# Kernel optimization log

Measured on AMD Instinct MI355X. Metric: run time of the kernel, lower is better.

## Reference

```python
import jax, jax.numpy as jnp
import numpy as np

N = 12288   # num_nodes
D = 128     # isize
K_TOP = 31  # k + 1, per top_k(similarities, self.k + 1)


def setup_inputs() -> dict:
    key = jax.random.key(0)
    features = jax.random.normal(key, (N, D), dtype=jnp.float32)
    eye = jnp.eye(D, dtype=jnp.float32)  # param_init: weight <- I, bias <- 0
    return {
        "features": features,
        "W1": eye,
        "b1": jnp.zeros((D,), jnp.float32),
        "W2": eye,
        "b2": jnp.zeros((D,), jnp.float32),
    }


def reference(features, W1, b1, W2, b2):
    # internal_forward: Linear -> ReLU -> Linear (nlayers=2, act='relu')
    h = jax.nn.relu(features @ W1.T + b1)
    h = h @ W2.T + b2
    # F.normalize(h, dim=1, p=2) with eps=1e-12
    hn = h / jnp.maximum(jnp.linalg.norm(h, axis=1, keepdims=True), 1e-12)
    # dense N x N cosine similarity
    sim = hn @ hn.T
    # top_k: keep top (k+1) entries per row, zero elsewhere; then apply_non_linearity='relu'
    vals, idx = jax.lax.top_k(sim, K_TOP)          # [N, K_TOP]
    rows = jnp.arange(sim.shape[0])[:, None]       # [N, 1]
    # relu(sim * mask) == scatter relu(top-k values) into a zero matrix
    out = jnp.zeros_like(sim).at[rows, idx].set(jax.nn.relu(vals))
    return out
```

## Files before the change

kernel.cpp:

```cpp
#include <hip/hip_runtime.h>
#include <stdint.h>
#include <math.h>

#define NN 12288
#define DD 128
#define KTOP 31
#define TILE 128
#define GB (NN / TILE)
#define TCAND 64
#define CCAP 128

typedef __attribute__((ext_vector_type(8))) short bf16x8;
typedef __attribute__((ext_vector_type(4))) float f32x4;

__device__ __forceinline__ unsigned short f2bf(float x) {
  unsigned int u = __float_as_uint(x);
  u += 0x7fffu + ((u >> 16) & 1u);
  return (unsigned short)(u >> 16);
}

__global__ __launch_bounds__(128)
void mlp_norm_kernel(const float* __restrict__ feat,
                     const float* __restrict__ W1, const float* __restrict__ b1,
                     const float* __restrict__ W2, const float* __restrict__ b2,
                     double* __restrict__ hn64, unsigned short* __restrict__ hnb) {
  __shared__ double bufA[8][DD];
  __shared__ double bufB[8][DD];
  __shared__ double mnorm[8];
  const int t = threadIdx.x;
  const int row0 = blockIdx.x * 8;

  #pragma unroll
  for (int rr = 0; rr < 8; ++rr)
    bufA[rr][t] = (double)feat[(size_t)(row0 + rr) * DD + t];
  __syncthreads();

  {
    double acc[8] = {0,0,0,0,0,0,0,0};
    const float* wrow = W1 + (size_t)t * DD;
    for (int k = 0; k < DD; ++k) {
      double w = (double)wrow[k];
      #pragma unroll
      for (int rr = 0; rr < 8; ++rr)
        acc[rr] = fma(w, bufA[rr][k], acc[rr]);
    }
    double bb = (double)b1[t];
    #pragma unroll
    for (int rr = 0; rr < 8; ++rr)
      bufB[rr][t] = fmax(acc[rr] + bb, 0.0);
  }
  __syncthreads();
  {
    double acc[8] = {0,0,0,0,0,0,0,0};
    const float* wrow = W2 + (size_t)t * DD;
    for (int k = 0; k < DD; ++k) {
      double w = (double)wrow[k];
      #pragma unroll
      for (int rr = 0; rr < 8; ++rr)
        acc[rr] = fma(w, bufB[rr][k], acc[rr]);
    }
    double bb = (double)b2[t];
    #pragma unroll
    for (int rr = 0; rr < 8; ++rr)
      bufA[rr][t] = acc[rr] + bb;
  }
  __syncthreads();

  const int lane = t & 63;
  const int w = t >> 6;
  #pragma unroll
  for (int r2 = 0; r2 < 4; ++r2) {
    int rr = w * 4 + r2;
    double x0 = bufA[rr][lane];
    double x1 = bufA[rr][lane + 64];
    double s = x0 * x0 + x1 * x1;
    #pragma unroll
    for (int d = 1; d < 64; d <<= 1)
      s += __shfl_xor(s, d);
    if (lane == 0) mnorm[rr] = fmax(sqrt(s), 1e-12);
  }
  __syncthreads();
  #pragma unroll
  for (int rr = 0; rr < 8; ++rr) {
    double v = bufA[rr][t] / mnorm[rr];
    hn64[(size_t)(row0 + rr) * DD + t] = v;
    hnb[(size_t)(row0 + rr) * DD + t] = f2bf((float)v);
  }
}

__device__ __forceinline__ int lunit(int c, int r, int q) {
  return c * 512 + r * 4 + ((q + (r >> 1)) & 3);
}

__global__ __launch_bounds__(256)
void gemm_kernel(const unsigned short* __restrict__ hnb,
                 unsigned short* __restrict__ simmat) {
  __shared__ __attribute__((aligned(16))) unsigned short At[16384];
  __shared__ __attribute__((aligned(16))) unsigned short Bt[16384];
  const int t = threadIdx.x;
  const int lane = t & 63;
  const int wv = t >> 6;
  const int bi = blockIdx.x / GB, bj = blockIdx.x % GB;
  const int r0 = bi * TILE, c0 = bj * TILE;

  #pragma unroll
  for (int i = 0; i < 8; ++i) {
    int u = i * 256 + t;
    int c = u >> 9, r = (u >> 2) & 127, g = u & 3;
    int q = (g - (r >> 1)) & 3;
    uint4 v = *(const uint4*)(hnb + (size_t)(r0 + r) * DD + c * 32 + q * 8);
    *(uint4*)(At + u * 8) = v;
  }
  #pragma unroll
  for (int i = 0; i < 8; ++i) {
    int u = i * 256 + t;
    int c = u >> 9, r = (u >> 2) & 127, g = u & 3;
    int q = (g - (r >> 1)) & 3;
    uint4 v = *(const uint4*)(hnb + (size_t)(c0 + r) * DD + c * 32 + q * 8);
    *(uint4*)(Bt + u * 8) = v;
  }
  __syncthreads();

  const int wr = (wv >> 1) * 64;
  const int wc = (wv & 1) * 64;
  const int m = lane & 15, quad = lane >> 4;

  f32x4 acc[4][4] = {};
  #pragma unroll
  for (int kc = 0; kc < 4; ++kc) {
    bf16x8 a[4], b[4];
    #pragma unroll
    for (int i = 0; i < 4; ++i)
      a[i] = *(const bf16x8*)(At + lunit(kc, wr + i * 16 + m, quad) * 8);
    #pragma unroll
    for (int j = 0; j < 4; ++j)
      b[j] = *(const bf16x8*)(Bt + lunit(kc, wc + j * 16 + m, quad) * 8);
    #pragma unroll
    for (int i = 0; i < 4; ++i)
      #pragma unroll
      for (int j = 0; j < 4; ++j)
        acc[i][j] = __builtin_amdgcn_mfma_f32_16x16x32_bf16(a[i], b[j], acc[i][j], 0, 0, 0);
  }

  const bool evenl = !(lane & 1);
  #pragma unroll
  for (int i = 0; i < 4; ++i)
    #pragma unroll
    for (int j = 0; j < 4; ++j)
      #pragma unroll
      for (int r = 0; r < 4; ++r) {
        float v = acc[i][j][r];
        float v2 = __shfl_xor(v, 1);
        if (evenl) {
          unsigned int pk = (unsigned int)f2bf(v) | ((unsigned int)f2bf(v2) << 16);
          int R = r0 + wr + i * 16 + quad * 4 + r;
          int C = c0 + wc + j * 16 + m;
          *(unsigned int*)(simmat + (size_t)R * NN + C) = pk;
        }
      }
}

#define PINS(P) { \
  unsigned p_ = (P); \
  _Pragma("unroll") \
  for (int i_ = 0; i_ < 7; ++i_) \
    L[i_] = (p_ > L[i_ + 1]) ? L[i_ + 1] : (L[i_] > p_ ? L[i_] : p_); \
  L[7] = L[7] > p_ ? L[7] : p_; }

__global__ __launch_bounds__(256)
void scan_rescore_kernel(const unsigned short* __restrict__ simmat,
                         const double* __restrict__ hn64,
                         float* __restrict__ resval, int* __restrict__ rescol) {
  __shared__ unsigned scand[4][CCAP];
  const int t = threadIdx.x, lane = t & 63, wv = t >> 6;
  const int row = blockIdx.x * 4 + wv;
  const unsigned short* srow = simmat + (size_t)row * NN;

  unsigned L[8] = {0, 0, 0, 0, 0, 0, 0, 0};
  for (int it = 0; it < NN / 512; ++it) {
    uint4 pk = *(const uint4*)(srow + it * 512 + lane * 8);
    const unsigned cb = it * 512 + lane * 8;
    unsigned wds[4] = {pk.x, pk.y, pk.z, pk.w};
    #pragma unroll
    for (int q = 0; q < 4; ++q) {
      unsigned b0 = wds[q] & 0xFFFFu, b1 = wds[q] >> 16;
      unsigned s0 = (b0 & 0x8000u) ? 0u : b0;
      unsigned s1 = (b1 & 0x8000u) ? 0u : b1;
      unsigned p0 = (s0 << 16) | (cb + 2 * q);
      unsigned p1 = (s1 << 16) | (cb + 2 * q + 1);
      if (p0 > L[0]) { PINS(p0) }
      if (p1 > L[0]) { PINS(p1) }
    }
  }

  unsigned lo = 0, hi = 0xFFFFu;
  while (lo < hi) {
    unsigned mid = (lo + hi + 1) >> 1;
    int c = 0;
    #pragma unroll
    for (int i = 0; i < 8; ++i) c += (int)((L[i] >> 16) >= mid);
    #pragma unroll
    for (int d = 1; d < 64; d <<= 1) c += __shfl_xor(c, d);
    if (c >= TCAND) lo = mid; else hi = mid - 1;
  }
  const unsigned thr = lo;

  int cl = 0;
  #pragma unroll
  for (int i = 0; i < 8; ++i) cl += (int)((L[i] >> 16) >= thr);
  int pre = cl;
  #pragma unroll
  for (int d = 1; d < 64; d <<= 1) {
    int y = __shfl_up(pre, d);
    if (lane >= d) pre += y;
  }
  const int total = __shfl(pre, 63);
  const int nc = total < CCAP ? total : CCAP;
  int slot = pre - cl;
  #pragma unroll
  for (int i = 0; i < 8; ++i) {
    if ((L[i] >> 16) >= thr) {
      if (slot < CCAP) scand[wv][slot] = L[i];
      ++slot;
    }
  }
  __syncthreads();

  const double* arow = hn64 + (size_t)row * DD;
  double rv0 = -1.0e300, rv1 = -1.0e300;
  int rc0 = 0x7fffffff, rc1 = 0x7fffffff;
  if (lane < nc) {
    const int col = (int)(scand[wv][lane] & 0xFFFFu);
    const double* brow = hn64 + (size_t)col * DD;
    double acc = 0.0;
    for (int k = 0; k < DD; k += 2) {
      double2 a2 = *(const double2*)(arow + k);
      double2 b2 = *(const double2*)(brow + k);
      acc = fma(a2.x, b2.x, acc);
      acc = fma(a2.y, b2.y, acc);
    }
    rv0 = acc; rc0 = col;
  }
  if (lane + 64 < nc) {
    const int col = (int)(scand[wv][lane + 64] & 0xFFFFu);
    const double* brow = hn64 + (size_t)col * DD;
    double acc = 0.0;
    for (int k = 0; k < DD; k += 2) {
      double2 a2 = *(const double2*)(arow + k);
      double2 b2 = *(const double2*)(brow + k);
      acc = fma(a2.x, b2.x, acc);
      acc = fma(a2.y, b2.y, acc);
    }
    rv1 = acc; rc1 = col;
  }

  for (int itk = 0; itk < KTOP; ++itk) {
    bool f = (rv0 > rv1) || (rv0 == rv1 && rc0 < rc1);
    double bv = f ? rv0 : rv1;
    int bc = f ? rc0 : rc1;
    #pragma unroll
    for (int d = 1; d < 64; d <<= 1) {
      double ov = __shfl_xor(bv, d);
      int    oc = __shfl_xor(bc, d);
      bool tk = (ov > bv) || (ov == bv && oc < bc);
      bv = tk ? ov : bv;
      bc = tk ? oc : bc;
    }
    if (lane == itk) {
      resval[(size_t)row * KTOP + itk] = (float)fmax(bv, 0.0);
      rescol[(size_t)row * KTOP + itk] = bc;
    }
    if (rv0 == bv && rc0 == bc) rv0 = -1.0e300;
    else if (rv1 == bv && rc1 == bc) rv1 = -1.0e300;
  }
}

__global__ __launch_bounds__(256)
void emit_kernel(const float* __restrict__ resval, const int* __restrict__ rescol,
                 float* __restrict__ out) {
  const int row = blockIdx.x, t = threadIdx.x;
  float v = 0.0f; int c = 0;
  if (t < KTOP) {
    v = resval[(size_t)row * KTOP + t];
    c = rescol[(size_t)row * KTOP + t];
  }
  float4* orow = (float4*)(out + (size_t)row * NN);
  const float4 z = {0.0f, 0.0f, 0.0f, 0.0f};
  #pragma unroll
  for (int i = 0; i < NN / 4 / 256; ++i)
    orow[i * 256 + t] = z;
  __syncthreads();
  if (t < KTOP) out[(size_t)row * NN + c] = v;
}

extern "C" void kernel_launch(void* const* d_in, const int* in_sizes, int n_in,
                              void* d_out, int out_size, void* d_ws, size_t ws_size,
                              hipStream_t stream) {
  const float* feat = (const float*)d_in[0];
  const float* W1 = (const float*)d_in[1];
  const float* b1 = (const float*)d_in[2];
  const float* W2 = (const float*)d_in[3];
  const float* b2 = (const float*)d_in[4];
  float* out = (float*)d_out;

  double* hn64 = (double*)d_ws;
  unsigned short* hnb = (unsigned short*)(hn64 + (size_t)NN * DD);
  float* resval = (float*)(hnb + (size_t)NN * DD);
  int* rescol = (int*)(resval + (size_t)NN * KTOP);

  unsigned short* simmat = (unsigned short*)d_out;

  mlp_norm_kernel<<<NN / 8, 128, 0, stream>>>(feat, W1, b1, W2, b2, hn64, hnb);
  gemm_kernel<<<GB * GB, 256, 0, stream>>>(hnb, simmat);
  scan_rescore_kernel<<<NN / 4, 256, 0, stream>>>(simmat, hn64, resval, rescol);
  emit_kernel<<<NN, 256, 0, stream>>>(resval, rescol, out);
}
```

Measured before the change: 1.025 ms.

## Filter similarity tiles in GEMM epilogue using per-row sampled thresholds

Adds a tau kernel that, for each row, computes similarities against a 512-row sample and takes the 24th-largest as a lower-bound threshold. The GEMM epilogue now appends only entries above that threshold to a per-row candidate buffer via atomics, instead of writing the full bf16 similarity matrix. The rescore kernel then reads these small candidate lists rather than scanning full rows. This removes the large simmat write and read traffic, at the cost of an extra kernel, atomic contention, and a fixed candidate capacity that could overflow or, if the sampled threshold is loose, miss true top-k entries.

```diff
diff --git a/kernel.cpp b/kernel.cpp
--- a/kernel.cpp
+++ b/kernel.cpp
@@ -9,6 +9,9 @@
 #define GB (NN / TILE)
 #define TCAND 64
 #define CCAP 128
+#define CAP 1536
+#define TAUN 512
+#define TAURANK 24
 
 typedef __attribute__((ext_vector_type(8))) short bf16x8;
 typedef __attribute__((ext_vector_type(4))) float f32x4;
@@ -17,6 +20,9 @@
   unsigned int u = __float_as_uint(x);
   u += 0x7fffu + ((u >> 16) & 1u);
   return (unsigned short)(u >> 16);
+}
+__device__ __forceinline__ float bf2f(unsigned int us) {
+  return __uint_as_float((us & 0xFFFFu) << 16);
 }
 
 __global__ __launch_bounds__(128)
@@ -88,13 +94,59 @@
   }
 }
 
+__global__ __launch_bounds__(256)
+void tau_kernel(const unsigned short* __restrict__ hnb,
+                unsigned short* __restrict__ tau) {
+  __shared__ unsigned short rowbuf[4 * DD];
+  const int t = threadIdx.x, lane = t & 63, wv = t >> 6;
+  const int row0 = blockIdx.x * 4;
+  ((unsigned*)rowbuf)[t] = ((const unsigned*)(hnb + (size_t)row0 * DD))[t];
+  __syncthreads();
+  const unsigned short* rb = rowbuf + wv * DD;
+
+  float acc[8] = {0,0,0,0,0,0,0,0};
+  for (int k8 = 0; k8 < DD; k8 += 8) {
+    float rv[8];
+    #pragma unroll
+    for (int e = 0; e < 8; ++e) rv[e] = bf2f(rb[k8 + e]);
+    #pragma unroll
+    for (int s = 0; s < 8; ++s) {
+      uint4 cv = *(const uint4*)(hnb + (size_t)(lane + 64 * s) * DD + k8);
+      unsigned wd[4] = {cv.x, cv.y, cv.z, cv.w};
+      #pragma unroll
+      for (int q = 0; q < 4; ++q) {
+        acc[s] = fmaf(bf2f(wd[q]), rv[2 * q], acc[s]);
+        acc[s] = fmaf(bf2f(wd[q] >> 16), rv[2 * q + 1], acc[s]);
+      }
+    }
+  }
+  unsigned key[8];
+  #pragma unroll
+  for (int s = 0; s < 8; ++s) {
+    unsigned bf = f2bf(acc[s]);
+    key[s] = (bf & 0x8000u) ? 0u : bf;
+  }
+  unsigned lo = 0, hi = 0xFFFFu;
+  while (lo < hi) {
+    unsigned mid = (lo + hi + 1) >> 1;
+    int c = 0;
+    #pragma unroll
+    for (int s = 0; s < 8; ++s) c += (int)(key[s] >= mid);
+    #pragma unroll
+    for (int d = 1; d < 64; d <<= 1) c += __shfl_xor(c, d);
+    if (c >= TAURANK) lo = mid; else hi = mid - 1;
+  }
+  if (lane == 0) tau[row0 + wv] = (unsigned short)(lo ? lo - 1 : 0);
+}
+
 __device__ __forceinline__ int lunit(int c, int r, int q) {
   return c * 512 + r * 4 + ((q + (r >> 1)) & 3);
 }
 
 __global__ __launch_bounds__(256)
-void gemm_kernel(const unsigned short* __restrict__ hnb,
-                 unsigned short* __restrict__ simmat) {
+void gemm_filter_kernel(const unsigned short* __restrict__ hnb,
+                        const unsigned short* __restrict__ tau,
+                        int* __restrict__ cnt, unsigned* __restrict__ cand) {
   __shared__ __attribute__((aligned(16))) unsigned short At[16384];
   __shared__ __attribute__((aligned(16))) unsigned short Bt[16384];
   const int t = threadIdx.x;
@@ -142,7 +194,13 @@
         acc[i][j] = __builtin_amdgcn_mfma_f32_16x16x32_bf16(a[i], b[j], acc[i][j], 0, 0, 0);
   }
 
-  const bool evenl = !(lane & 1);
+  unsigned short tr[4][4];
+  #pragma unroll
+  for (int i = 0; i < 4; ++i)
+    #pragma unroll
+    for (int r = 0; r < 4; ++r)
+      tr[i][r] = tau[r0 + wr + i * 16 + quad * 4 + r];
+
   #pragma unroll
   for (int i = 0; i < 4; ++i)
     #pragma unroll
@@ -150,47 +208,32 @@
       #pragma unroll
       for (int r = 0; r < 4; ++r) {
         float v = acc[i][j][r];
-        float v2 = __shfl_xor(v, 1);
-        if (evenl) {
-          unsigned int pk = (unsigned int)f2bf(v) | ((unsigned int)f2bf(v2) << 16);
+        unsigned bf = f2bf(v);
+        unsigned key = (bf & 0x8000u) ? 0u : bf;
+        if (key >= (unsigned)tr[i][r]) {
           int R = r0 + wr + i * 16 + quad * 4 + r;
           int C = c0 + wc + j * 16 + m;
-          *(unsigned int*)(simmat + (size_t)R * NN + C) = pk;
+          int idx = atomicAdd(&cnt[R], 1);
+          if (idx < CAP) cand[(size_t)R * CAP + idx] = (key << 16) | (unsigned)C;
         }
       }
 }
 
-#define PINS(P) { \
-  unsigned p_ = (P); \
-  _Pragma("unroll") \
-  for (int i_ = 0; i_ < 7; ++i_) \
-    L[i_] = (p_ > L[i_ + 1]) ? L[i_ + 1] : (L[i_] > p_ ? L[i_] : p_); \
-  L[7] = L[7] > p_ ? L[7] : p_; }
-
 __global__ __launch_bounds__(256)
-void scan_rescore_kernel(const unsigned short* __restrict__ simmat,
-                         const double* __restrict__ hn64,
-                         float* __restrict__ resval, int* __restrict__ rescol) {
+void rescore_kernel(const unsigned* __restrict__ cand, const int* __restrict__ cnt,
+                    const double* __restrict__ hn64,
+                    float* __restrict__ resval, int* __restrict__ rescol) {
   __shared__ unsigned scand[4][CCAP];
   const int t = threadIdx.x, lane = t & 63, wv = t >> 6;
   const int row = blockIdx.x * 4 + wv;
-  const unsigned short* srow = simmat + (size_t)row * NN;
-
-  unsigned L[8] = {0, 0, 0, 0, 0, 0, 0, 0};
-  for (int it = 0; it < NN / 512; ++it) {
-    uint4 pk = *(const uint4*)(srow + it * 512 + lane * 8);
-    const unsigned cb = it * 512 + lane * 8;
-    unsigned wds[4] = {pk.x, pk.y, pk.z, pk.w};
-    #pragma unroll
-    for (int q = 0; q < 4; ++q) {
-      unsigned b0 = wds[q] & 0xFFFFu, b1 = wds[q] >> 16;
-      unsigned s0 = (b0 & 0x8000u) ? 0u : b0;
-      unsigned s1 = (b1 & 0x8000u) ? 0u : b1;
-      unsigned p0 = (s0 << 16) | (cb + 2 * q);
-      unsigned p1 = (s1 << 16) | (cb + 2 * q + 1);
-      if (p0 > L[0]) { PINS(p0) }
-      if (p1 > L[0]) { PINS(p1) }
-    }
+  int n = cnt[row];
+  n = n > CAP ? CAP : n;
+
+  unsigned ck[CAP / 64];
+  #pragma unroll
+  for (int i = 0; i < CAP / 64; ++i) {
+    int idx = lane + 64 * i;
+    ck[i] = (idx < n) ? cand[(size_t)row * CAP + idx] : 0u;
   }
 
   unsigned lo = 0, hi = 0xFFFFu;
@@ -198,7 +241,7 @@
     unsigned mid = (lo + hi + 1) >> 1;
     int c = 0;
     #pragma unroll
-    for (int i = 0; i < 8; ++i) c += (int)((L[i] >> 16) >= mid);
+    for (int i = 0; i < CAP / 64; ++i) c += (int)((ck[i] >> 16) >= mid);
     #pragma unroll
     for (int d = 1; d < 64; d <<= 1) c += __shfl_xor(c, d);
     if (c >= TCAND) lo = mid; else hi = mid - 1;
@@ -207,7 +250,8 @@
 
   int cl = 0;
   #pragma unroll
-  for (int i = 0; i < 8; ++i) cl += (int)((L[i] >> 16) >= thr);
+  for (int i = 0; i < CAP / 64; ++i)
+    cl += (int)((lane + 64 * i < n) && ((ck[i] >> 16) >= thr));
   int pre = cl;
   #pragma unroll
   for (int d = 1; d < 64; d <<= 1) {
@@ -218,9 +262,9 @@
   const int nc = total < CCAP ? total : CCAP;
   int slot = pre - cl;
   #pragma unroll
-  for (int i = 0; i < 8; ++i) {
-    if ((L[i] >> 16) >= thr) {
-      if (slot < CCAP) scand[wv][slot] = L[i];
+  for (int i = 0; i < CAP / 64; ++i) {
+    if ((lane + 64 * i < n) && ((ck[i] >> 16) >= thr)) {
+      if (slot < CCAP) scand[wv][slot] = ck[i];
       ++slot;
     }
   }
@@ -307,11 +351,14 @@
   unsigned short* hnb = (unsigned short*)(hn64 + (size_t)NN * DD);
   float* resval = (float*)(hnb + (size_t)NN * DD);
   int* rescol = (int*)(resval + (size_t)NN * KTOP);
-
-  unsigned short* simmat = (unsigned short*)d_out;
-
+  unsigned* cand = (unsigned*)(rescol + (size_t)NN * KTOP);
+  int* cnt = (int*)(cand + (size_t)NN * CAP);
+  unsigned short* tau = (unsigned short*)(cnt + NN);
+
+  hipMemsetAsync(cnt, 0, NN * sizeof(int), stream);
   mlp_norm_kernel<<<NN / 8, 128, 0, stream>>>(feat, W1, b1, W2, b2, hn64, hnb);
-  gemm_kernel<<<GB * GB, 256, 0, stream>>>(hnb, simmat);
-  scan_rescore_kernel<<<NN / 4, 256, 0, stream>>>(simmat, hn64, resval, rescol);
+  tau_kernel<<<NN / 4, 256, 0, stream>>>(hnb, tau);
+  gemm_filter_kernel<<<GB * GB, 256, 0, stream>>>(hnb, tau, cnt, cand);
+  rescore_kernel<<<NN / 4, 256, 0, stream>>>(cand, cnt, hn64, resval, rescol);
   emit_kernel<<<NN, 256, 0, stream>>>(resval, rescol, out);
 }
```

Result: slower. 2.403 ms (+134.4%).
